# Kernel optimization log

Hardware: AMD Instinct MI355X
Metric: run time of the kernel (lower is better)

## Reference

```python
import jax, jax.numpy as jnp
import numpy as np

N, E, D_IN, D_H, D_OUT = 50000, 600000, 128, 128, 1


def setup_inputs() -> dict:
    key = jax.random.key(0)
    ks = jax.random.split(key, 12)
    s = 1.0 / np.sqrt(D_H)
    inp = {
        "x": jax.random.normal(ks[0], (N, D_IN), dtype=jnp.float32),
        "edge_index": jax.random.randint(ks[1], (2, E), 0, N, dtype=jnp.int64),
        # GCNConv layer weights (in->h, h->h, h->h)
        "W0": jax.random.normal(ks[2], (D_IN, D_H), dtype=jnp.float32) * s,
        "b0": jnp.zeros((D_H,), dtype=jnp.float32),
        "W1": jax.random.normal(ks[3], (D_H, D_H), dtype=jnp.float32) * s,
        "b1": jnp.zeros((D_H,), dtype=jnp.float32),
        "W2": jax.random.normal(ks[4], (D_H, D_H), dtype=jnp.float32) * s,
        "b2": jnp.zeros((D_H,), dtype=jnp.float32),
        # MLP head
        "mlp_w1": jax.random.normal(ks[5], (D_H, D_H), dtype=jnp.float32) * s,
        "mlp_b1": jnp.zeros((D_H,), dtype=jnp.float32),
        "mlp_w2": jax.random.normal(ks[6], (D_H, D_OUT), dtype=jnp.float32) * s,
        "mlp_b2": jnp.zeros((D_OUT,), dtype=jnp.float32),
    }
    return inp


def reference(x, edge_index, W0, b0, W1, b1, W2, b2, mlp_w1, mlp_b1, mlp_w2, mlp_b2):
    n = x.shape[0]
    loop = jnp.arange(n, dtype=edge_index.dtype)
    # add self-loops (PyG GCNConv default)
    src = jnp.concatenate([edge_index[0], loop])
    dst = jnp.concatenate([edge_index[1], loop])
    # symmetric normalization: deg counts incoming edges incl. self-loop
    deg = jax.ops.segment_sum(jnp.ones(src.shape, dtype=x.dtype), dst, num_segments=n)
    dinv = jax.lax.rsqrt(deg)  # deg >= 1 due to self-loops
    norm = (dinv[src] * dinv[dst])[:, None]  # [E+N, 1]

    def gcn_conv(h, W, b):
        h = h @ W                       # [N, d]
        msg = h[src] * norm             # gather + scale, [E+N, d]
        return jax.ops.segment_sum(msg, dst, num_segments=n) + b

    # num_layers=3: first two convs with ReLU (dropout is identity in eval)
    h = jax.nn.relu(gcn_conv(x, W0, b0))
    h = jax.nn.relu(gcn_conv(h, W1, b1))
    h = gcn_conv(h, W2, b2)
    # MLP head (dropout identity in eval)
    h = jax.nn.relu(h @ mlp_w1 + mlp_b1)
    return h @ mlp_w2 + mlp_b2
```

## Files before the change

kernel.cpp:

```cpp
#include <hip/hip_runtime.h>
#include <hip/hip_fp16.h>

constexpr int D = 128;

typedef _Float16 half8 __attribute__((ext_vector_type(8)));
typedef float f32x4 __attribute__((ext_vector_type(4)));


__global__ void k_zero(int4* __restrict__ p, int n4) {
    int i = blockIdx.x * 256 + threadIdx.x;
    if (i < n4) p[i] = make_int4(0, 0, 0, 0);
}


__global__ void k_count(const int* __restrict__ dst, int* __restrict__ cnt, int E) {
    int e = blockIdx.x * 256 + threadIdx.x;
    if (e < E) atomicAdd(&cnt[dst[e]], 1);
}

__global__ __launch_bounds__(256) void k_deg_stats(const int* __restrict__ cnt,
                                                   float* __restrict__ dinv,
                                                   int* __restrict__ bsum, int n) {
    __shared__ int sm[256];
    int tid = threadIdx.x;
    int i = blockIdx.x * 256 + tid;
    int c = (i < n) ? cnt[i] : 0;
    if (i < n) dinv[i] = rsqrtf((float)(c + 1));
    sm[tid] = c;
    __syncthreads();
    for (int off = 128; off > 0; off >>= 1) {
        if (tid < off) sm[tid] += sm[tid + off];
        __syncthreads();
    }
    if (tid == 0) bsum[blockIdx.x] = sm[0];
}

__global__ __launch_bounds__(256) void k_local_scan2(const int* __restrict__ cnt,
                                                     const int* __restrict__ bsum, int nb,
                                                     int* __restrict__ rowptr,
                                                     int* __restrict__ cursor, int n) {
    __shared__ int sb[256];
    __shared__ int sm[256];
    int tid = threadIdx.x;
    int bid = blockIdx.x;
    int bv = (tid < nb) ? bsum[tid] : 0;
    sb[tid] = bv;
    __syncthreads();
    for (int off = 1; off < 256; off <<= 1) {
        int t = (tid >= off) ? sb[tid - off] : 0;
        __syncthreads();
        sb[tid] += t;
        __syncthreads();
    }
    int blockoff = (bid > 0) ? sb[bid - 1] : 0;
    int i = bid * 256 + tid;
    int v = (i < n) ? cnt[i] : 0;
    sm[tid] = v;
    __syncthreads();
    for (int off = 1; off < 256; off <<= 1) {
        int t = (tid >= off) ? sm[tid - off] : 0;
        __syncthreads();
        sm[tid] += t;
        __syncthreads();
    }
    if (i < n) {
        int rp = blockoff + sm[tid] - v;
        rowptr[i] = rp;
        cursor[i] = rp;
    }
    if (bid == 0 && tid == 0) rowptr[n] = sb[nb - 1];
}


template <typename IdxT>
__global__ __launch_bounds__(256) void k_prep(
    const int* __restrict__ src, const int* __restrict__ dst, int* __restrict__ cursor,
    IdxT* __restrict__ csr, int E, const float* __restrict__ x,
    const float* __restrict__ dinv, __half* __restrict__ xh, int n4,
    const float* __restrict__ W0, const float* __restrict__ W1,
    const float* __restrict__ W2, const float* __restrict__ M1,
    const float* __restrict__ b2, const float* __restrict__ c1,
    __half* __restrict__ Wf0, __half* __restrict__ Wf1, __half* __restrict__ Wfp,
    float* __restrict__ cp) {
    int T = gridDim.x * 256;
    int gid = blockIdx.x * 256 + threadIdx.x;

    for (int e = gid; e < E; e += T) {
        int s = src[e], d = dst[e];
        int p = atomicAdd(&cursor[d], 1);
        csr[p] = (IdxT)s;
    }

    for (int i = gid; i < n4; i += T) {
        float4 v = reinterpret_cast<const float4*>(x)[i];
        float dd = dinv[i >> 5];
        __half ho[4] = {__float2half(v.x * dd), __float2half(v.y * dd),
                        __float2half(v.z * dd), __float2half(v.w * dd)};
        reinterpret_cast<uint2*>(xh)[i] = *reinterpret_cast<uint2*>(ho);
    }

    for (int q = gid; q < 2 * 16384; q += T) {
        int m = q >> 14;
        int idx = q & 16383;
        int j = idx & 7;
        int l = (idx >> 3) & 63;
        int c = (idx >> 9) & 7;
        int kk = (idx >> 12) & 3;
        int row = kk * 32 + (l >> 4) * 8 + j;
        int col = c * 16 + (l & 15);
        const float* W = (m == 0) ? W0 : W1;
        __half* Wf = (m == 0) ? Wf0 : Wf1;
        Wf[idx] = __float2half(W[row * 128 + col]);
    }

    for (int idx = gid; idx < 16384; idx += T) {
        int j = idx & 7;
        int l = (idx >> 3) & 63;
        int c = (idx >> 9) & 7;
        int kk = (idx >> 12) & 3;
        int row = kk * 32 + (l >> 4) * 8 + j;
        int col = c * 16 + (l & 15);
        float acc = 0.f;
        for (int k = 0; k < 128; ++k)
            acc = fmaf(W2[row * 128 + k], M1[k * 128 + col], acc);
        Wfp[idx] = __float2half(acc);
    }

    if (gid < 128) {
        float acc = c1[gid];
        for (int k = 0; k < 128; ++k) acc = fmaf(b2[k], M1[k * 128 + gid], acc);
        cp[gid] = acc;
    }
}


__device__ inline void accm(float* a, uint4 g, float m) {
    float2 p0 = __half22float2(*reinterpret_cast<const __half2*>(&g.x));
    float2 p1 = __half22float2(*reinterpret_cast<const __half2*>(&g.y));
    float2 p2 = __half22float2(*reinterpret_cast<const __half2*>(&g.z));
    float2 p3 = __half22float2(*reinterpret_cast<const __half2*>(&g.w));
    a[0] = fmaf(m, p0.x, a[0]);
    a[1] = fmaf(m, p0.y, a[1]);
    a[2] = fmaf(m, p1.x, a[2]);
    a[3] = fmaf(m, p1.y, a[3]);
    a[4] = fmaf(m, p2.x, a[4]);
    a[5] = fmaf(m, p2.y, a[5]);
    a[6] = fmaf(m, p3.x, a[6]);
    a[7] = fmaf(m, p3.y, a[7]);
}

template <typename IdxT>
__global__ __launch_bounds__(256) void k_agg_h4(const uint4* __restrict__ Ah4,
                                                const int* __restrict__ rowptr,
                                                const IdxT* __restrict__ csr,
                                                const float* __restrict__ dinv,
                                                uint4* __restrict__ outh4, int n) {
    int wv = threadIdx.x >> 6;
    int lane = threadIdx.x & 63;
    int half = lane >> 5;
    int l31 = lane & 31;
    int qg2 = (lane >> 4) & 1;
    int fl = lane & 15;
    int i = blockIdx.x * 8 + wv * 2 + half;
    if (i >= n) i = n - 1;

    float a[8];
#pragma unroll
    for (int j = 0; j < 8; ++j) a[j] = 0.f;
    int beg = rowptr[i], end = rowptr[i + 1];
    for (int base = beg; base < end; base += 32) {
        int c2 = end - base;
        if (c2 > 32) c2 = 32;
        int idxv = (base + l31 < end) ? (int)csr[base + l31] : 0;
        for (int e = 0; e < c2; e += 8) {
            int k0 = e + qg2;
            int k1 = e + qg2 + 2;
            int k2 = e + qg2 + 4;
            int k3 = e + qg2 + 6;
            int s0 = __shfl(idxv, half * 32 + k0);
            int s1 = __shfl(idxv, half * 32 + k1);
            int s2 = __shfl(idxv, half * 32 + k2);
            int s3 = __shfl(idxv, half * 32 + k3);
            uint4 g0 = Ah4[s0 * 16 + fl];
            uint4 g1 = Ah4[s1 * 16 + fl];
            uint4 g2 = Ah4[s2 * 16 + fl];
            uint4 g3 = Ah4[s3 * 16 + fl];
            float m0 = (k0 < c2) ? 1.f : 0.f;
            float m1 = (k1 < c2) ? 1.f : 0.f;
            float m2 = (k2 < c2) ? 1.f : 0.f;
            float m3 = (k3 < c2) ? 1.f : 0.f;
            accm(a, g0, m0);
            accm(a, g1, m1);
            accm(a, g2, m2);
            accm(a, g3, m3);
        }
    }
#pragma unroll
    for (int j = 0; j < 8; ++j) a[j] += __shfl_xor(a[j], 16);
    if (qg2 == 0) {
        uint4 gs = Ah4[i * 16 + fl];
        accm(a, gs, 1.f);
        float di = dinv[i];
        __half ho[8];
#pragma unroll
        for (int j = 0; j < 8; ++j) ho[j] = __float2half(di * a[j]);
        outh4[i * 16 + fl] = *reinterpret_cast<const uint4*>(ho);
    }
}


template <int MODE>
__global__ __launch_bounds__(256) void k_gemm_mfma(const __half* __restrict__ A,
                                                   const __half* __restrict__ Wf,
                                                   const float* __restrict__ bias,
                                                   const float* __restrict__ dinv,
                                                   const float* __restrict__ m2,
                                                   const float* __restrict__ m2b,
                                                   void* __restrict__ outv, int n) {
    int tid = threadIdx.x;
    int w = tid >> 6;
    int l = tid & 63;
    int r0 = blockIdx.x * 64 + w * 16;
    int arow = r0 + (l & 15);
    if (arow > n - 1) arow = n - 1;
    int kb = (l >> 4) * 8;

    f32x4 acc[8];
#pragma unroll
    for (int c = 0; c < 8; ++c) acc[c] = (f32x4){0.f, 0.f, 0.f, 0.f};

#pragma unroll
    for (int kk = 0; kk < 4; ++kk) {
        half8 a = *reinterpret_cast<const half8*>(&A[arow * 128 + kk * 32 + kb]);
#pragma unroll
        for (int c = 0; c < 8; ++c) {
            half8 b = *reinterpret_cast<const half8*>(&Wf[((kk * 8 + c) * 64 + l) * 8]);
            acc[c] = __builtin_amdgcn_mfma_f32_16x16x32_f16(a, b, acc[c], 0, 0, 0);
        }
    }

    float bv[8];
#pragma unroll
    for (int c = 0; c < 8; ++c) bv[c] = bias[c * 16 + (l & 15)];

    if (MODE == 0) {
        __half* outh = (__half*)outv;
#pragma unroll
        for (int reg = 0; reg < 4; ++reg) {
            int r = r0 + (l >> 4) * 4 + reg;
            if (r < n) {
                float dr = dinv[r];
#pragma unroll
                for (int c = 0; c < 8; ++c) {
                    float v = dr * fmaxf(acc[c][reg] + bv[c], 0.f);
                    outh[r * 128 + c * 16 + (l & 15)] = __float2half(v);
                }
            }
        }
    } else {
        float* out = (float*)outv;
        float mv[8];
#pragma unroll
        for (int c = 0; c < 8; ++c) mv[c] = m2[c * 16 + (l & 15)];
        float m2bv = m2b[0];
#pragma unroll
        for (int reg = 0; reg < 4; ++reg) {
            float p = 0.f;
#pragma unroll
            for (int c = 0; c < 8; ++c)
                p = fmaf(fmaxf(acc[c][reg] + bv[c], 0.f), mv[c], p);
            p += __shfl_xor(p, 1);
            p += __shfl_xor(p, 2);
            p += __shfl_xor(p, 4);
            p += __shfl_xor(p, 8);
            int r = r0 + (l >> 4) * 4 + reg;
            if ((l & 15) == 0 && r < n) out[r] = p + m2bv;
        }
    }
}


extern "C" void kernel_launch(void* const* d_in, const int* in_sizes, int n_in,
                              void* d_out, int out_size, void* d_ws, size_t ws_size,
                              hipStream_t stream) {
    const float* x = (const float*)d_in[0];
    const int* ei = (const int*)d_in[1];
    const float* W0 = (const float*)d_in[2];
    const float* b0 = (const float*)d_in[3];
    const float* W1 = (const float*)d_in[4];
    const float* b1 = (const float*)d_in[5];
    const float* W2 = (const float*)d_in[6];
    const float* b2 = (const float*)d_in[7];
    const float* M1 = (const float*)d_in[8];
    const float* c1 = (const float*)d_in[9];
    const float* m2 = (const float*)d_in[10];
    const float* m2b = (const float*)d_in[11];
    float* out = (float*)d_out;

    int N = in_sizes[0] / D;
    int E = in_sizes[1] / 2;
    const int* src = ei;
    const int* dst = ei + E;

    char* ws = (char*)d_ws;
    size_t off = 0;
    auto alloc = [&](size_t bytes) -> void* {
        void* p = ws + off;
        off += (bytes + 255) & ~(size_t)255;
        return p;
    };

    int gN = (N + 255) / 256;
    int gAgg = (N + 7) / 8;
    int gGemm = (N + 63) / 64;
    int nElem4 = N * D / 4;

    __half* xh = (__half*)alloc((size_t)N * D * 2);
    __half* tbuf = (__half*)alloc((size_t)N * D * 2);
    __half* gbuf = (__half*)alloc((size_t)N * D * 2);
    int* cnt = (int*)alloc((size_t)N * 4);
    float* dinv = (float*)alloc((size_t)N * 4);
    int* rowptr = (int*)alloc((size_t)(N + 1) * 4);
    int* cursor = (int*)alloc((size_t)N * 4);
    void* csr = alloc((size_t)E * 4);
    float* cp = (float*)alloc((size_t)D * 4);
    __half* Wf0 = (__half*)alloc((size_t)D * D * 2);
    __half* Wf1 = (__half*)alloc((size_t)D * D * 2);
    __half* Wfp = (__half*)alloc((size_t)D * D * 2);
    int* bsum = (int*)alloc((size_t)gN * 4);

    bool small_idx = (N <= 65535);

    int zc = (N + 3) / 4;
    k_zero<<<(zc + 255) / 256, 256, 0, stream>>>((int4*)cnt, zc);
    k_count<<<(E + 255) / 256, 256, 0, stream>>>(dst, cnt, E);
    k_deg_stats<<<gN, 256, 0, stream>>>(cnt, dinv, bsum, N);
    k_local_scan2<<<gN, 256, 0, stream>>>(cnt, bsum, gN, rowptr, cursor, N);
    if (small_idx)
        k_prep<ushort><<<2048, 256, 0, stream>>>(src, dst, cursor, (ushort*)csr, E, x,
                                                 dinv, xh, nElem4, W0, W1, W2, M1, b2,
                                                 c1, Wf0, Wf1, Wfp, cp);
    else
        k_prep<uint><<<2048, 256, 0, stream>>>(src, dst, cursor, (uint*)csr, E, x, dinv,
                                               xh, nElem4, W0, W1, W2, M1, b2, c1, Wf0,
                                               Wf1, Wfp, cp);

    auto agg = [&](const __half* in_h, __half* out_t) {
        if (small_idx)
            k_agg_h4<ushort><<<gAgg, 256, 0, stream>>>((const uint4*)in_h, rowptr,
                                                       (const ushort*)csr, dinv,
                                                       (uint4*)out_t, N);
        else
            k_agg_h4<uint><<<gAgg, 256, 0, stream>>>((const uint4*)in_h, rowptr,
                                                     (const uint*)csr, dinv,
                                                     (uint4*)out_t, N);
    };

    agg(xh, tbuf);
    k_gemm_mfma<0><<<gGemm, 256, 0, stream>>>(tbuf, Wf0, b0, dinv, nullptr, nullptr,
                                              gbuf, N);
    agg(gbuf, tbuf);
    k_gemm_mfma<0><<<gGemm, 256, 0, stream>>>(tbuf, Wf1, b1, dinv, nullptr, nullptr,
                                              gbuf, N);
    agg(gbuf, tbuf);
    k_gemm_mfma<1><<<gGemm, 256, 0, stream>>>(tbuf, Wfp, cp, dinv, m2, m2b, out, N);
}
```

Before: 180.6 us.

## Fuse sparse aggregation with MFMA GEMM per 32-row tile via LDS

Merges each aggregation kernel with the following MFMA GEMM into one kernel. Each block aggregates 32 rows into a swizzled LDS tile, then four waves split the tile into two row halves and two column halves for the GEMM. This removes the fp16 intermediate buffer's global write and reread and halves the number of launches per layer. In exchange, blocks now serialise gather latency and GEMM behind a barrier, and the MLP-head mode needs an extra LDS reduction across the column halves.

```diff
diff --git a/kernel.cpp b/kernel.cpp
--- a/kernel.cpp
+++ b/kernel.cpp
@@ -149,132 +149,135 @@
     a[7] = fmaf(m, p3.y, a[7]);
 }
 
-template <typename IdxT>
-__global__ __launch_bounds__(256) void k_agg_h4(const uint4* __restrict__ Ah4,
-                                                const int* __restrict__ rowptr,
-                                                const IdxT* __restrict__ csr,
-                                                const float* __restrict__ dinv,
-                                                uint4* __restrict__ outh4, int n) {
-    int wv = threadIdx.x >> 6;
-    int lane = threadIdx.x & 63;
+template <int MODE, typename IdxT>
+__global__ __launch_bounds__(256) void k_fused(const uint4* __restrict__ Ah4,
+                                               const int* __restrict__ rowptr,
+                                               const IdxT* __restrict__ csr,
+                                               const float* __restrict__ dinv,
+                                               const __half* __restrict__ Wf,
+                                               const float* __restrict__ bias,
+                                               const float* __restrict__ m2,
+                                               const float* __restrict__ m2b,
+                                               void* __restrict__ outv, int n) {
+    __shared__ uint4 Ht[32 * 16];
+    __shared__ float ph[2][32];
+    int tid = threadIdx.x;
+    int wv = tid >> 6;
+    int lane = tid & 63;
+    int r0 = blockIdx.x * 32;
+
     int half = lane >> 5;
     int l31 = lane & 31;
     int qg2 = (lane >> 4) & 1;
     int fl = lane & 15;
-    int i = blockIdx.x * 8 + wv * 2 + half;
-    if (i >= n) i = n - 1;
-
-    float a[8];
-#pragma unroll
-    for (int j = 0; j < 8; ++j) a[j] = 0.f;
-    int beg = rowptr[i], end = rowptr[i + 1];
-    for (int base = beg; base < end; base += 32) {
-        int c2 = end - base;
-        if (c2 > 32) c2 = 32;
-        int idxv = (base + l31 < end) ? (int)csr[base + l31] : 0;
-        for (int e = 0; e < c2; e += 8) {
-            int k0 = e + qg2;
-            int k1 = e + qg2 + 2;
-            int k2 = e + qg2 + 4;
-            int k3 = e + qg2 + 6;
-            int s0 = __shfl(idxv, half * 32 + k0);
-            int s1 = __shfl(idxv, half * 32 + k1);
-            int s2 = __shfl(idxv, half * 32 + k2);
-            int s3 = __shfl(idxv, half * 32 + k3);
-            uint4 g0 = Ah4[s0 * 16 + fl];
-            uint4 g1 = Ah4[s1 * 16 + fl];
-            uint4 g2 = Ah4[s2 * 16 + fl];
-            uint4 g3 = Ah4[s3 * 16 + fl];
-            float m0 = (k0 < c2) ? 1.f : 0.f;
-            float m1 = (k1 < c2) ? 1.f : 0.f;
-            float m2 = (k2 < c2) ? 1.f : 0.f;
-            float m3 = (k3 < c2) ? 1.f : 0.f;
-            accm(a, g0, m0);
-            accm(a, g1, m1);
-            accm(a, g2, m2);
-            accm(a, g3, m3);
-        }
-    }
-#pragma unroll
-    for (int j = 0; j < 8; ++j) a[j] += __shfl_xor(a[j], 16);
-    if (qg2 == 0) {
-        uint4 gs = Ah4[i * 16 + fl];
-        accm(a, gs, 1.f);
-        float di = dinv[i];
-        __half ho[8];
-#pragma unroll
-        for (int j = 0; j < 8; ++j) ho[j] = __float2half(di * a[j]);
-        outh4[i * 16 + fl] = *reinterpret_cast<const uint4*>(ho);
-    }
-}
-
-
-template <int MODE>
-__global__ __launch_bounds__(256) void k_gemm_mfma(const __half* __restrict__ A,
-                                                   const __half* __restrict__ Wf,
-                                                   const float* __restrict__ bias,
-                                                   const float* __restrict__ dinv,
-                                                   const float* __restrict__ m2,
-                                                   const float* __restrict__ m2b,
-                                                   void* __restrict__ outv, int n) {
-    int tid = threadIdx.x;
-    int w = tid >> 6;
-    int l = tid & 63;
-    int r0 = blockIdx.x * 64 + w * 16;
-    int arow = r0 + (l & 15);
-    if (arow > n - 1) arow = n - 1;
-    int kb = (l >> 4) * 8;
-
-    f32x4 acc[8];
-#pragma unroll
-    for (int c = 0; c < 8; ++c) acc[c] = (f32x4){0.f, 0.f, 0.f, 0.f};
+    for (int it = 0; it < 4; ++it) {
+        int lr = wv * 8 + it * 2 + half;
+        int i = r0 + lr;
+        if (i >= n) i = n - 1;
+        float a[8];
+#pragma unroll
+        for (int j = 0; j < 8; ++j) a[j] = 0.f;
+        int beg = rowptr[i], end = rowptr[i + 1];
+        for (int base = beg; base < end; base += 32) {
+            int c2 = end - base;
+            if (c2 > 32) c2 = 32;
+            int idxv = (base + l31 < end) ? (int)csr[base + l31] : 0;
+            for (int e = 0; e < c2; e += 8) {
+                int k0 = e + qg2;
+                int k1 = e + qg2 + 2;
+                int k2 = e + qg2 + 4;
+                int k3 = e + qg2 + 6;
+                int s0 = __shfl(idxv, half * 32 + k0);
+                int s1 = __shfl(idxv, half * 32 + k1);
+                int s2 = __shfl(idxv, half * 32 + k2);
+                int s3 = __shfl(idxv, half * 32 + k3);
+                uint4 g0 = Ah4[s0 * 16 + fl];
+                uint4 g1 = Ah4[s1 * 16 + fl];
+                uint4 g2 = Ah4[s2 * 16 + fl];
+                uint4 g3 = Ah4[s3 * 16 + fl];
+                float m0 = (k0 < c2) ? 1.f : 0.f;
+                float m1 = (k1 < c2) ? 1.f : 0.f;
+                float m2_ = (k2 < c2) ? 1.f : 0.f;
+                float m3 = (k3 < c2) ? 1.f : 0.f;
+                accm(a, g0, m0);
+                accm(a, g1, m1);
+                accm(a, g2, m2_);
+                accm(a, g3, m3);
+            }
+        }
+#pragma unroll
+        for (int j = 0; j < 8; ++j) a[j] += __shfl_xor(a[j], 16);
+        if (qg2 == 0) {
+            uint4 gs = Ah4[i * 16 + fl];
+            accm(a, gs, 1.f);
+            float di = dinv[i];
+            __half ho[8];
+#pragma unroll
+            for (int j = 0; j < 8; ++j) ho[j] = __float2half(di * a[j]);
+            Ht[lr * 16 + (fl ^ (lr & 7))] = *reinterpret_cast<const uint4*>(ho);
+        }
+    }
+    __syncthreads();
+
+    int w4 = wv & 1;
+    int ch = wv >> 1;
+    int rr = w4 * 16 + (lane & 15);
+
+    f32x4 acc[4];
+#pragma unroll
+    for (int c = 0; c < 4; ++c) acc[c] = (f32x4){0.f, 0.f, 0.f, 0.f};
 
 #pragma unroll
     for (int kk = 0; kk < 4; ++kk) {
-        half8 a = *reinterpret_cast<const half8*>(&A[arow * 128 + kk * 32 + kb]);
-#pragma unroll
-        for (int c = 0; c < 8; ++c) {
-            half8 b = *reinterpret_cast<const half8*>(&Wf[((kk * 8 + c) * 64 + l) * 8]);
+        int bk = kk * 4 + (lane >> 4);
+        half8 a = *reinterpret_cast<const half8*>(&Ht[rr * 16 + (bk ^ (rr & 7))]);
+#pragma unroll
+        for (int c = 0; c < 4; ++c) {
+            int gc = ch * 4 + c;
+            half8 b = *reinterpret_cast<const half8*>(&Wf[((kk * 8 + gc) * 64 + lane) * 8]);
             acc[c] = __builtin_amdgcn_mfma_f32_16x16x32_f16(a, b, acc[c], 0, 0, 0);
         }
     }
 
-    float bv[8];
-#pragma unroll
-    for (int c = 0; c < 8; ++c) bv[c] = bias[c * 16 + (l & 15)];
+    float bv[4];
+#pragma unroll
+    for (int c = 0; c < 4; ++c) bv[c] = bias[ch * 64 + c * 16 + (lane & 15)];
 
     if (MODE == 0) {
         __half* outh = (__half*)outv;
 #pragma unroll
         for (int reg = 0; reg < 4; ++reg) {
-            int r = r0 + (l >> 4) * 4 + reg;
+            int r = r0 + w4 * 16 + (lane >> 4) * 4 + reg;
             if (r < n) {
                 float dr = dinv[r];
 #pragma unroll
-                for (int c = 0; c < 8; ++c) {
+                for (int c = 0; c < 4; ++c) {
                     float v = dr * fmaxf(acc[c][reg] + bv[c], 0.f);
-                    outh[r * 128 + c * 16 + (l & 15)] = __float2half(v);
+                    outh[r * 128 + ch * 64 + c * 16 + (lane & 15)] = __float2half(v);
                 }
             }
         }
     } else {
         float* out = (float*)outv;
-        float mv[8];
-#pragma unroll
-        for (int c = 0; c < 8; ++c) mv[c] = m2[c * 16 + (l & 15)];
-        float m2bv = m2b[0];
+        float mv[4];
+#pragma unroll
+        for (int c = 0; c < 4; ++c) mv[c] = m2[ch * 64 + c * 16 + (lane & 15)];
 #pragma unroll
         for (int reg = 0; reg < 4; ++reg) {
             float p = 0.f;
 #pragma unroll
-            for (int c = 0; c < 8; ++c)
+            for (int c = 0; c < 4; ++c)
                 p = fmaf(fmaxf(acc[c][reg] + bv[c], 0.f), mv[c], p);
             p += __shfl_xor(p, 1);
             p += __shfl_xor(p, 2);
             p += __shfl_xor(p, 4);
             p += __shfl_xor(p, 8);
-            int r = r0 + (l >> 4) * 4 + reg;
-            if ((l & 15) == 0 && r < n) out[r] = p + m2bv;
+            if ((lane & 15) == 0) ph[ch][w4 * 16 + (lane >> 4) * 4 + reg] = p;
+        }
+        __syncthreads();
+        if (tid < 32) {
+            int r = r0 + tid;
+            if (r < n) out[r] = ph[0][tid] + ph[1][tid] + m2b[0];
         }
     }
 }
@@ -311,13 +314,12 @@
     };
 
     int gN = (N + 255) / 256;
-    int gAgg = (N + 7) / 8;
-    int gGemm = (N + 63) / 64;
+    int gFused = (N + 31) / 32;
     int nElem4 = N * D / 4;
 
     __half* xh = (__half*)alloc((size_t)N * D * 2);
-    __half* tbuf = (__half*)alloc((size_t)N * D * 2);
-    __half* gbuf = (__half*)alloc((size_t)N * D * 2);
+    __half* bufA = (__half*)alloc((size_t)N * D * 2);
+    __half* bufB = (__half*)alloc((size_t)N * D * 2);
     int* cnt = (int*)alloc((size_t)N * 4);
     float* dinv = (float*)alloc((size_t)N * 4);
     int* rowptr = (int*)alloc((size_t)(N + 1) * 4);
@@ -345,23 +347,26 @@
                                                xh, nElem4, W0, W1, W2, M1, b2, c1, Wf0,
                                                Wf1, Wfp, cp);
 
-    auto agg = [&](const __half* in_h, __half* out_t) {
+    auto fused0 = [&](const __half* in_h, const __half* Wf, const float* b,
+                      __half* out_h) {
         if (small_idx)
-            k_agg_h4<ushort><<<gAgg, 256, 0, stream>>>((const uint4*)in_h, rowptr,
-                                                       (const ushort*)csr, dinv,
-                                                       (uint4*)out_t, N);
+            k_fused<0, ushort><<<gFused, 256, 0, stream>>>(
+                (const uint4*)in_h, rowptr, (const ushort*)csr, dinv, Wf, b, nullptr,
+                nullptr, out_h, N);
         else
-            k_agg_h4<uint><<<gAgg, 256, 0, stream>>>((const uint4*)in_h, rowptr,
-                                                     (const uint*)csr, dinv,
-                                                     (uint4*)out_t, N);
+            k_fused<0, uint><<<gFused, 256, 0, stream>>>(
+                (const uint4*)in_h, rowptr, (const uint*)csr, dinv, Wf, b, nullptr,
+                nullptr, out_h, N);
     };
 
-    agg(xh, tbuf);
-    k_gemm_mfma<0><<<gGemm, 256, 0, stream>>>(tbuf, Wf0, b0, dinv, nullptr, nullptr,
-                                              gbuf, N);
-    agg(gbuf, tbuf);
-    k_gemm_mfma<0><<<gGemm, 256, 0, stream>>>(tbuf, Wf1, b1, dinv, nullptr, nullptr,
-                                              gbuf, N);
-    agg(gbuf, tbuf);
-    k_gemm_mfma<1><<<gGemm, 256, 0, stream>>>(tbuf, Wfp, cp, dinv, m2, m2b, out, N);
-}
+    fused0(xh, Wf0, b0, bufA);
+    fused0(bufA, Wf1, b1, bufB);
+    if (small_idx)
+        k_fused<1, ushort><<<gFused, 256, 0, stream>>>(
+            (const uint4*)bufB, rowptr, (const ushort*)csr, dinv, Wfp, cp, m2, m2b, out,
+            N);
+    else
+        k_fused<1, uint><<<gFused, 256, 0, stream>>>(
+            (const uint4*)bufB, rowptr, (const uint*)csr, dinv, Wfp, cp, m2, m2b, out,
+            N);
+}
```

After: 172.1 us, median of 2. 4.7% less time.
